# Kernel tuning notes

Hardware: AMD Instinct MI355X
Metric: run time of the kernel (lower is better)

## Reference

```python
import jax, jax.numpy as jnp
import numpy as np
from jax import lax

B, T, I, H, L = 256, 512, 156, 128, 32


def setup_inputs() -> dict:
    key = jax.random.key(0)
    ks = jax.random.split(key, 16)
    kb = 1.0 / np.sqrt(H)  # torch default LSTM/Linear init bound

    def u(k, shape, bound):
        return jax.random.uniform(k, shape, minval=-bound, maxval=bound, dtype=jnp.float32)

    return {
        "motion": jax.random.normal(ks[0], (B, T, I), dtype=jnp.float32),
        "eps": jax.random.normal(ks[1], (B, L), dtype=jnp.float32),
        # encoder LSTM (gate order i,f,g,o; b = b_ih + b_hh folded together)
        "enc_Wih": u(ks[2], (4 * H, I), kb),
        "enc_Whh": u(ks[3], (4 * H, H), kb),
        "enc_b": u(ks[4], (4 * H,), kb),
        "mu_W": u(ks[5], (L, H), kb),
        "mu_b": u(ks[6], (L,), kb),
        "var_W": u(ks[7], (L, H), kb),
        "var_b": u(ks[8], (L,), kb),
        # decoder
        "dec_fc_W": u(ks[9], (H, L), 1.0 / np.sqrt(L)),
        "dec_fc_b": u(ks[10], (H,), 1.0 / np.sqrt(L)),
        "dec_Wih": u(ks[11], (4 * H, H), kb),
        "dec_Whh": u(ks[12], (4 * H, H), kb),
        "dec_b": u(ks[13], (4 * H,), kb),
        "out_W": u(ks[14], (I, H), kb),
        "out_b": u(ks[15], (I,), kb),
    }


def _cell(gates, c):
    # PyTorch LSTM gate layout: [i, f, g, o] along the 4H axis
    i, f, g, o = jnp.split(gates, 4, axis=-1)
    c_new = jax.nn.sigmoid(f) * c + jax.nn.sigmoid(i) * jnp.tanh(g)
    h_new = jax.nn.sigmoid(o) * jnp.tanh(c_new)
    return h_new, c_new


def reference(motion, eps, enc_Wih, enc_Whh, enc_b, mu_W, mu_b, var_W, var_b,
              dec_fc_W, dec_fc_b, dec_Wih, dec_Whh, dec_b, out_W, out_b):
    b, t, _ = motion.shape

    # ---- encoder LSTM: single scan over time, keep only final hidden ----
    def enc_step(carry, x_t):
        h, c = carry
        gates = x_t @ enc_Wih.T + h @ enc_Whh.T + enc_b
        h, c = _cell(gates, c)
        return (h, c), None

    h0 = jnp.zeros((b, H), motion.dtype)
    c0 = jnp.zeros((b, H), motion.dtype)
    (h_fin, _), _ = lax.scan(enc_step, (h0, c0), jnp.swapaxes(motion, 0, 1))

    mu = h_fin @ mu_W.T + mu_b          # [B, L]
    logvar = h_fin @ var_W.T + var_b    # [B, L] ('var' in the torch code)

    # ---- reparameterize ----
    z = mu + eps * jnp.exp(0.5 * logvar)

    # ---- decoder: input at each step is the previous hidden state ----
    dh0 = z @ dec_fc_W.T + dec_fc_b     # [B, H]
    dc0 = jnp.zeros((b, H), motion.dtype)

    def dec_step(carry, _):
        h, c = carry
        gates = h @ dec_Wih.T + h @ dec_Whh.T + dec_b
        h, c = _cell(gates, c)
        return (h, c), h

    _, hs = lax.scan(dec_step, (dh0, dc0), None, length=t)  # [T, B, H]
    recon = jnp.einsum('tbh,oh->bto', hs, out_W) + out_b    # [B, T, I]

    # ---- losses ----
    rec_loss = jnp.mean((recon - motion) ** 2)
    kl_loss = -0.5 * jnp.sum(1.0 + logvar - mu ** 2 - jnp.exp(logvar))
    total = rec_loss + kl_loss
    return recon, mu, logvar, total
```

## Files before the change

kernel.cpp:

```cpp
#include <hip/hip_runtime.h>
#include <hip/hip_fp16.h>

#define B_ 256
#define T_ 512
#define I_ 156
#define H_ 128
#define L_ 32
#define G_ 512

typedef _Float16 half_t;
typedef _Float16 h2_t __attribute__((ext_vector_type(2)));

union U8 { uint4 u; h2_t h2[4]; };

__device__ __forceinline__ float fdot2(h2_t a, h2_t b, float c) {
#if __has_builtin(__builtin_amdgcn_fdot2)
  return __builtin_amdgcn_fdot2(a, b, c, false);
#else
  return c + (float)a[0] * (float)b[0] + (float)a[1] * (float)b[1];
#endif
}

__device__ __forceinline__ h2_t pk2(float a, float b) {
  h2_t r; r[0] = (half_t)a; r[1] = (half_t)b; return r;
}

__device__ __forceinline__ float sigf(float x) { return 1.0f / (1.0f + __expf(-x)); }
__device__ __forceinline__ float tanhf_(float x) {
  x = fminf(fmaxf(x, -20.f), 20.f);
  float e = __expf(2.f * x);
  return (e - 1.f) / (e + 1.f);
}

__global__ __launch_bounds__(512, 2) void enc_kernel(
    const float* __restrict__ motion, const float* __restrict__ eps,
    const float* __restrict__ Wih, const float* __restrict__ Whh,
    const float* __restrict__ bv,
    const float* __restrict__ muW, const float* __restrict__ mub,
    const float* __restrict__ varW, const float* __restrict__ varb,
    const float* __restrict__ fcW, const float* __restrict__ fcb,
    float* __restrict__ dout, float* __restrict__ dh0,
    float* __restrict__ accums)
{
  const int j = threadIdx.x;
  const int b = blockIdx.x;

  __shared__ U8 xs[20];
  __shared__ U8 hs[16];
  __shared__ float gl[G_];
  __shared__ float hf[H_];
  __shared__ float mulv[64];
  __shared__ float zs[L_];

  h2_t wih[80];
  h2_t whh[64];
  {
    const float2* r = (const float2*)(Wih + j * I_);
#pragma unroll
    for (int k = 0; k < 78; ++k) { float2 w = r[k]; wih[k] = pk2(w.x, w.y); }
    wih[78] = pk2(0.f, 0.f); wih[79] = pk2(0.f, 0.f);
    const float2* r2 = (const float2*)(Whh + j * H_);
#pragma unroll
    for (int k = 0; k < 64; ++k) { float2 w = r2[k]; whh[k] = pk2(w.x, w.y); }
  }
  const float bj = bv[j];

  float creg = 0.f, hreg = 0.f;
  if (j < 64) { ((h2_t*)hs)[j] = pk2(0.f, 0.f); }

  const float2* mrow = (const float2*)(motion + (size_t)b * T_ * I_);

  for (int t = 0; t < T_; ++t) {
    if (j < 80) {
      h2_t v = pk2(0.f, 0.f);
      if (j < 78) { float2 m = mrow[t * 78 + j]; v = pk2(m.x, m.y); }
      ((h2_t*)xs)[j] = v;
    }
    __syncthreads();
    float acc = bj;
#pragma unroll
    for (int c = 0; c < 20; ++c) {
      U8 xv = xs[c];
      acc = fdot2(wih[4*c+0], xv.h2[0], acc);
      acc = fdot2(wih[4*c+1], xv.h2[1], acc);
      acc = fdot2(wih[4*c+2], xv.h2[2], acc);
      acc = fdot2(wih[4*c+3], xv.h2[3], acc);
    }
#pragma unroll
    for (int c = 0; c < 16; ++c) {
      U8 hv = hs[c];
      acc = fdot2(whh[4*c+0], hv.h2[0], acc);
      acc = fdot2(whh[4*c+1], hv.h2[1], acc);
      acc = fdot2(whh[4*c+2], hv.h2[2], acc);
      acc = fdot2(whh[4*c+3], hv.h2[3], acc);
    }
    gl[j] = acc;
    __syncthreads();
    if (j < H_) {
      float ig = gl[j], fg = gl[j + H_], gg = gl[j + 2*H_], og = gl[j + 3*H_];
      creg = sigf(fg) * creg + sigf(ig) * tanhf_(gg);
      hreg = sigf(og) * tanhf_(creg);
      ((half_t*)hs)[j] = (half_t)hreg;
    }
    __syncthreads();
  }

  if (j < H_) hf[j] = hreg;
  __syncthreads();

  if (j < 64) {
    const float* wr = (j < L_) ? (muW + j * H_) : (varW + (j - L_) * H_);
    float a = (j < L_) ? mub[j] : varb[j - L_];
#pragma unroll 8
    for (int k = 0; k < H_; ++k) a += wr[k] * hf[k];
    mulv[j] = a;
    if (j < L_) dout[(size_t)B_*T_*I_ + b * L_ + j] = a;
    else        dout[(size_t)B_*T_*I_ + B_*L_ + b * L_ + (j - L_)] = a;
  }
  __syncthreads();

  if (j < L_) {
    float mu = mulv[j], lv = mulv[j + L_];
    float z = mu + eps[b * L_ + j] * __expf(0.5f * lv);
    zs[j] = z;
    float kt = 1.f + lv - mu * mu - __expf(lv);
#pragma unroll
    for (int off = 16; off > 0; off >>= 1) kt += __shfl_down(kt, off, 64);
    if (j == 0) atomicAdd(&accums[1], kt);
  }
  __syncthreads();

  if (j < H_) {
    const float* wr = fcW + j * L_;
    float a = fcb[j];
#pragma unroll
    for (int l = 0; l < L_; ++l) a += wr[l] * zs[l];
    dh0[b * H_ + j] = a;
  }
}

__global__ __launch_bounds__(512, 2) void dec_kernel(
    const float* __restrict__ motion,
    const float* __restrict__ Wih, const float* __restrict__ Whh,
    const float* __restrict__ bv,
    const float* __restrict__ oW, const float* __restrict__ ob,
    const float* __restrict__ dh0,
    float* __restrict__ dout, float* __restrict__ accums)
{
  const int j = threadIdx.x;
  const int b = blockIdx.x;

  __shared__ U8 hs[16];
  __shared__ float gl[G_];
  __shared__ float red[8];

  h2_t wd[64];
  {
    const float2* r1 = (const float2*)(Wih + j * H_);
    const float2* r2 = (const float2*)(Whh + j * H_);
#pragma unroll
    for (int k = 0; k < 64; ++k) {
      float2 a = r1[k], c = r2[k];
      wd[k] = pk2(a.x + c.x, a.y + c.y);
    }
  }
  const float bj = bv[j];

  h2_t wo[64];
  float obj = 0.f;
  if (j < I_) {
    const float2* r = (const float2*)(oW + j * H_);
#pragma unroll
    for (int k = 0; k < 64; ++k) { float2 w = r[k]; wo[k] = pk2(w.x, w.y); }
    obj = ob[j];
  } else {
#pragma unroll
    for (int k = 0; k < 64; ++k) wo[k] = pk2(0.f, 0.f);
  }

  float creg = 0.f, hreg = 0.f;
  if (j < H_) {
    hreg = dh0[b * H_ + j];
    ((half_t*)hs)[j] = (half_t)hreg;
  }
  __syncthreads();

  const float* mrow = motion + (size_t)b * T_ * I_;
  float* rrow = dout + (size_t)b * T_ * I_;
  float rl = 0.f;

  for (int t = 0; t < T_; ++t) {
    float acc = bj;
#pragma unroll
    for (int c = 0; c < 16; ++c) {
      U8 hv = hs[c];
      acc = fdot2(wd[4*c+0], hv.h2[0], acc);
      acc = fdot2(wd[4*c+1], hv.h2[1], acc);
      acc = fdot2(wd[4*c+2], hv.h2[2], acc);
      acc = fdot2(wd[4*c+3], hv.h2[3], acc);
    }
    gl[j] = acc;
    __syncthreads();
    if (j < H_) {
      float ig = gl[j], fg = gl[j + H_], gg = gl[j + 2*H_], og = gl[j + 3*H_];
      creg = sigf(fg) * creg + sigf(ig) * tanhf_(gg);
      hreg = sigf(og) * tanhf_(creg);
      ((half_t*)hs)[j] = (half_t)hreg;
    }
    __syncthreads();
    if (j < I_) {
      float r = obj;
#pragma unroll
      for (int c = 0; c < 16; ++c) {
        U8 hv = hs[c];
        r = fdot2(wo[4*c+0], hv.h2[0], r);
        r = fdot2(wo[4*c+1], hv.h2[1], r);
        r = fdot2(wo[4*c+2], hv.h2[2], r);
        r = fdot2(wo[4*c+3], hv.h2[3], r);
      }
      rrow[t * I_ + j] = r;
      float d = r - mrow[t * I_ + j];
      rl += d * d;
    }
  }

  float v = rl;
#pragma unroll
  for (int off = 32; off > 0; off >>= 1) v += __shfl_down(v, off, 64);
  if ((j & 63) == 0) red[j >> 6] = v;
  __syncthreads();
  if (j == 0) {
    float s = 0.f;
#pragma unroll
    for (int w = 0; w < 8; ++w) s += red[w];
    atomicAdd(&accums[0], s);
  }
}

__global__ void init_kernel(float* accums) {
  if (threadIdx.x < 2) accums[threadIdx.x] = 0.f;
}

__global__ void fin_kernel(const float* __restrict__ accums, float* __restrict__ dout) {
  if (threadIdx.x == 0) {
    float rec = accums[0] / (float)((size_t)B_ * T_ * I_);
    float kl = -0.5f * accums[1];
    dout[(size_t)B_*T_*I_ + 2 * B_ * L_] = rec + kl;
  }
}

extern "C" void kernel_launch(void* const* d_in, const int* in_sizes, int n_in,
                              void* d_out, int out_size, void* d_ws, size_t ws_size,
                              hipStream_t stream) {
  const float* motion = (const float*)d_in[0];
  const float* eps    = (const float*)d_in[1];
  const float* eWih   = (const float*)d_in[2];
  const float* eWhh   = (const float*)d_in[3];
  const float* eb     = (const float*)d_in[4];
  const float* muW    = (const float*)d_in[5];
  const float* mub    = (const float*)d_in[6];
  const float* varW   = (const float*)d_in[7];
  const float* varb   = (const float*)d_in[8];
  const float* fcW    = (const float*)d_in[9];
  const float* fcb    = (const float*)d_in[10];
  const float* dWih   = (const float*)d_in[11];
  const float* dWhh   = (const float*)d_in[12];
  const float* db     = (const float*)d_in[13];
  const float* oW     = (const float*)d_in[14];
  const float* obv    = (const float*)d_in[15];
  float* out = (float*)d_out;
  float* accums = (float*)d_ws;
  float* dh0    = (float*)d_ws + 16;

  hipLaunchKernelGGL(init_kernel, dim3(1), dim3(64), 0, stream, accums);
  hipLaunchKernelGGL(enc_kernel, dim3(B_), dim3(512), 0, stream,
                     motion, eps, eWih, eWhh, eb, muW, mub, varW, varb, fcW, fcb,
                     out, dh0, accums);
  hipLaunchKernelGGL(dec_kernel, dim3(B_), dim3(512), 0, stream,
                     motion, dWih, dWhh, db, oW, obv, dh0, out, accums);
  hipLaunchKernelGGL(fin_kernel, dim3(1), dim3(64), 0, stream, accums, out);
}
```

Measured before the change: 1.437 ms.

## Split LSTM gate dot products across 1024 threads and pipeline decoder output projection

Both kernels move to 1024-thread blocks. The encoder splits each gate's input and hidden dot products across two thread halves, sums the halves in the cell update, and prefetches the next timestep's motion row into a double buffer. The decoder gives the output projection to its own half of threads, which computes step t-1's reconstruction while the other half computes the gates for step t, taking that projection off the serial chain and removing one barrier wait per step. In exchange, launch bounds of 4 blocks of 1024 threads squeeze per-thread registers (each thread still holds 64 packed decoder weights), which risks spills or lower occupancy, and each step adds a partial-sum read through shared memory.

```diff
diff --git a/kernel.cpp b/kernel.cpp
--- a/kernel.cpp
+++ b/kernel.cpp
@@ -32,7 +32,7 @@
   return (e - 1.f) / (e + 1.f);
 }
 
-__global__ __launch_bounds__(512, 2) void enc_kernel(
+__global__ __launch_bounds__(1024, 4) void enc_kernel(
     const float* __restrict__ motion, const float* __restrict__ eps,
     const float* __restrict__ Wih, const float* __restrict__ Whh,
     const float* __restrict__ bv,
@@ -42,104 +42,125 @@
     float* __restrict__ dout, float* __restrict__ dh0,
     float* __restrict__ accums)
 {
-  const int j = threadIdx.x;
-  const int b = blockIdx.x;
-
-  __shared__ U8 xs[20];
-  __shared__ U8 hs[16];
-  __shared__ float gl[G_];
+  const int tid  = threadIdx.x;
+  const int part = tid >> 9;
+  const int j    = tid & 511;
+  const int b    = blockIdx.x;
+
+  __shared__ h2_t xs[2][80];
+  __shared__ h2_t hs[64];
+  __shared__ float gl2[2][G_];
   __shared__ float hf[H_];
   __shared__ float mulv[64];
   __shared__ float zs[L_];
 
-  h2_t wih[80];
-  h2_t whh[64];
+  h2_t wih[40];
+  h2_t whh[32];
   {
-    const float2* r = (const float2*)(Wih + j * I_);
-#pragma unroll
-    for (int k = 0; k < 78; ++k) { float2 w = r[k]; wih[k] = pk2(w.x, w.y); }
-    wih[78] = pk2(0.f, 0.f); wih[79] = pk2(0.f, 0.f);
-    const float2* r2 = (const float2*)(Whh + j * H_);
-#pragma unroll
-    for (int k = 0; k < 64; ++k) { float2 w = r2[k]; whh[k] = pk2(w.x, w.y); }
-  }
-  const float bj = bv[j];
+    const int cbase = part * 80;
+    const float* wr = Wih + (size_t)j * I_;
+#pragma unroll
+    for (int k = 0; k < 40; ++k) {
+      int c0 = cbase + 2 * k;
+      float a = (c0     < I_) ? wr[c0]     : 0.f;
+      float c = (c0 + 1 < I_) ? wr[c0 + 1] : 0.f;
+      wih[k] = pk2(a, c);
+    }
+    const float2* r2 = (const float2*)(Whh + (size_t)j * H_ + part * 64);
+#pragma unroll
+    for (int k = 0; k < 32; ++k) { float2 w = r2[k]; whh[k] = pk2(w.x, w.y); }
+  }
+
+  float cb0 = 0.f, cb1 = 0.f, cb2 = 0.f, cb3 = 0.f;
+  if (tid < H_) {
+    cb0 = bv[tid]; cb1 = bv[tid + H_]; cb2 = bv[tid + 2*H_]; cb3 = bv[tid + 3*H_];
+  }
 
   float creg = 0.f, hreg = 0.f;
-  if (j < 64) { ((h2_t*)hs)[j] = pk2(0.f, 0.f); }
+  if (tid < 64) hs[tid] = pk2(0.f, 0.f);
+  if (tid < 4)  xs[tid >> 1][78 + (tid & 1)] = pk2(0.f, 0.f);
 
   const float2* mrow = (const float2*)(motion + (size_t)b * T_ * I_);
-
+  const bool loader = (part == 1) && (j < 78);
+  if (loader) { float2 m = mrow[j]; xs[0][j] = pk2(m.x, m.y); }
+  __syncthreads();
+
+  int cur = 0;
+  float2 xreg;
   for (int t = 0; t < T_; ++t) {
-    if (j < 80) {
-      h2_t v = pk2(0.f, 0.f);
-      if (j < 78) { float2 m = mrow[t * 78 + j]; v = pk2(m.x, m.y); }
-      ((h2_t*)xs)[j] = v;
-    }
+    if (loader && t + 1 < T_) xreg = mrow[(t + 1) * 78 + j];
+
+    float a0 = 0.f, a1 = 0.f, a2 = 0.f, a3 = 0.f;
+    const U8* xv = (const U8*)&xs[cur][part * 40];
+#pragma unroll
+    for (int c = 0; c < 10; ++c) {
+      U8 v = xv[c];
+      a0 = fdot2(wih[4*c+0], v.h2[0], a0);
+      a1 = fdot2(wih[4*c+1], v.h2[1], a1);
+      a2 = fdot2(wih[4*c+2], v.h2[2], a2);
+      a3 = fdot2(wih[4*c+3], v.h2[3], a3);
+    }
+    const U8* hv = (const U8*)&hs[part * 32];
+#pragma unroll
+    for (int c = 0; c < 8; ++c) {
+      U8 v = hv[c];
+      a0 = fdot2(whh[4*c+0], v.h2[0], a0);
+      a1 = fdot2(whh[4*c+1], v.h2[1], a1);
+      a2 = fdot2(whh[4*c+2], v.h2[2], a2);
+      a3 = fdot2(whh[4*c+3], v.h2[3], a3);
+    }
+    gl2[part][j] = (a0 + a1) + (a2 + a3);
+    if (loader && t + 1 < T_) xs[cur ^ 1][j] = pk2(xreg.x, xreg.y);
     __syncthreads();
-    float acc = bj;
-#pragma unroll
-    for (int c = 0; c < 20; ++c) {
-      U8 xv = xs[c];
-      acc = fdot2(wih[4*c+0], xv.h2[0], acc);
-      acc = fdot2(wih[4*c+1], xv.h2[1], acc);
-      acc = fdot2(wih[4*c+2], xv.h2[2], acc);
-      acc = fdot2(wih[4*c+3], xv.h2[3], acc);
-    }
-#pragma unroll
-    for (int c = 0; c < 16; ++c) {
-      U8 hv = hs[c];
-      acc = fdot2(whh[4*c+0], hv.h2[0], acc);
-      acc = fdot2(whh[4*c+1], hv.h2[1], acc);
-      acc = fdot2(whh[4*c+2], hv.h2[2], acc);
-      acc = fdot2(whh[4*c+3], hv.h2[3], acc);
-    }
-    gl[j] = acc;
-    __syncthreads();
-    if (j < H_) {
-      float ig = gl[j], fg = gl[j + H_], gg = gl[j + 2*H_], og = gl[j + 3*H_];
+
+    if (tid < H_) {
+      float ig = gl2[0][tid]         + gl2[1][tid]         + cb0;
+      float fg = gl2[0][tid +   H_]  + gl2[1][tid +   H_]  + cb1;
+      float gg = gl2[0][tid + 2*H_]  + gl2[1][tid + 2*H_]  + cb2;
+      float og = gl2[0][tid + 3*H_]  + gl2[1][tid + 3*H_]  + cb3;
       creg = sigf(fg) * creg + sigf(ig) * tanhf_(gg);
       hreg = sigf(og) * tanhf_(creg);
-      ((half_t*)hs)[j] = (half_t)hreg;
+      ((half_t*)hs)[tid] = (half_t)hreg;
     }
     __syncthreads();
-  }
-
-  if (j < H_) hf[j] = hreg;
-  __syncthreads();
-
-  if (j < 64) {
-    const float* wr = (j < L_) ? (muW + j * H_) : (varW + (j - L_) * H_);
-    float a = (j < L_) ? mub[j] : varb[j - L_];
+    cur ^= 1;
+  }
+
+  if (tid < H_) hf[tid] = hreg;
+  __syncthreads();
+
+  if (tid < 64) {
+    const float* wr = (tid < L_) ? (muW + tid * H_) : (varW + (tid - L_) * H_);
+    float a = (tid < L_) ? mub[tid] : varb[tid - L_];
 #pragma unroll 8
     for (int k = 0; k < H_; ++k) a += wr[k] * hf[k];
-    mulv[j] = a;
-    if (j < L_) dout[(size_t)B_*T_*I_ + b * L_ + j] = a;
-    else        dout[(size_t)B_*T_*I_ + B_*L_ + b * L_ + (j - L_)] = a;
-  }
-  __syncthreads();
-
-  if (j < L_) {
-    float mu = mulv[j], lv = mulv[j + L_];
-    float z = mu + eps[b * L_ + j] * __expf(0.5f * lv);
-    zs[j] = z;
+    mulv[tid] = a;
+    if (tid < L_) dout[(size_t)B_*T_*I_ + b * L_ + tid] = a;
+    else          dout[(size_t)B_*T_*I_ + B_*L_ + b * L_ + (tid - L_)] = a;
+  }
+  __syncthreads();
+
+  if (tid < L_) {
+    float mu = mulv[tid], lv = mulv[tid + L_];
+    float z = mu + eps[b * L_ + tid] * __expf(0.5f * lv);
+    zs[tid] = z;
     float kt = 1.f + lv - mu * mu - __expf(lv);
 #pragma unroll
     for (int off = 16; off > 0; off >>= 1) kt += __shfl_down(kt, off, 64);
-    if (j == 0) atomicAdd(&accums[1], kt);
-  }
-  __syncthreads();
-
-  if (j < H_) {
-    const float* wr = fcW + j * L_;
-    float a = fcb[j];
+    if (tid == 0) atomicAdd(&accums[1], kt);
+  }
+  __syncthreads();
+
+  if (tid < H_) {
+    const float* wr = fcW + tid * L_;
+    float a = fcb[tid];
 #pragma unroll
     for (int l = 0; l < L_; ++l) a += wr[l] * zs[l];
-    dh0[b * H_ + j] = a;
-  }
-}
-
-__global__ __launch_bounds__(512, 2) void dec_kernel(
+    dh0[b * H_ + tid] = a;
+  }
+}
+
+__global__ __launch_bounds__(1024, 4) void dec_kernel(
     const float* __restrict__ motion,
     const float* __restrict__ Wih, const float* __restrict__ Whh,
     const float* __restrict__ bv,
@@ -147,92 +168,110 @@
     const float* __restrict__ dh0,
     float* __restrict__ dout, float* __restrict__ accums)
 {
-  const int j = threadIdx.x;
-  const int b = blockIdx.x;
-
-  __shared__ U8 hs[16];
+  const int tid  = threadIdx.x;
+  const int part = tid >> 9;
+  const int j    = tid & 511;
+  const int b    = blockIdx.x;
+
+  __shared__ h2_t hs[64];
   __shared__ float gl[G_];
-  __shared__ float red[8];
-
-  h2_t wd[64];
-  {
-    const float2* r1 = (const float2*)(Wih + j * H_);
-    const float2* r2 = (const float2*)(Whh + j * H_);
+  __shared__ float red[16];
+
+  h2_t wv[64];
+  float bj = 0.f;
+  if (part == 0) {
+    const float2* r1 = (const float2*)(Wih + (size_t)j * H_);
+    const float2* r2 = (const float2*)(Whh + (size_t)j * H_);
 #pragma unroll
     for (int k = 0; k < 64; ++k) {
       float2 a = r1[k], c = r2[k];
-      wd[k] = pk2(a.x + c.x, a.y + c.y);
-    }
-  }
-  const float bj = bv[j];
-
-  h2_t wo[64];
-  float obj = 0.f;
-  if (j < I_) {
-    const float2* r = (const float2*)(oW + j * H_);
-#pragma unroll
-    for (int k = 0; k < 64; ++k) { float2 w = r[k]; wo[k] = pk2(w.x, w.y); }
-    obj = ob[j];
-  } else {
-#pragma unroll
-    for (int k = 0; k < 64; ++k) wo[k] = pk2(0.f, 0.f);
+      wv[k] = pk2(a.x + c.x, a.y + c.y);
+    }
+    bj = bv[j];
+  } else if (j < I_) {
+    const float2* r = (const float2*)(oW + (size_t)j * H_);
+#pragma unroll
+    for (int k = 0; k < 64; ++k) { float2 w = r[k]; wv[k] = pk2(w.x, w.y); }
+    bj = ob[j];
   }
 
   float creg = 0.f, hreg = 0.f;
-  if (j < H_) {
-    hreg = dh0[b * H_ + j];
-    ((half_t*)hs)[j] = (half_t)hreg;
-  }
-  __syncthreads();
-
-  const float* mrow = motion + (size_t)b * T_ * I_;
-  float* rrow = dout + (size_t)b * T_ * I_;
+  if (tid < H_) {
+    hreg = dh0[b * H_ + tid];
+    ((half_t*)hs)[tid] = (half_t)hreg;
+  }
+  __syncthreads();
+
+  const float* mr = motion + (size_t)b * T_ * I_;
+  float* rr = dout + (size_t)b * T_ * I_;
   float rl = 0.f;
 
   for (int t = 0; t < T_; ++t) {
-    float acc = bj;
-#pragma unroll
-    for (int c = 0; c < 16; ++c) {
-      U8 hv = hs[c];
-      acc = fdot2(wd[4*c+0], hv.h2[0], acc);
-      acc = fdot2(wd[4*c+1], hv.h2[1], acc);
-      acc = fdot2(wd[4*c+2], hv.h2[2], acc);
-      acc = fdot2(wd[4*c+3], hv.h2[3], acc);
-    }
-    gl[j] = acc;
+    if (part == 0) {
+      float a0 = 0.f, a1 = 0.f, a2 = 0.f, a3 = 0.f;
+      const U8* hv = (const U8*)hs;
+#pragma unroll
+      for (int c = 0; c < 16; ++c) {
+        U8 v = hv[c];
+        a0 = fdot2(wv[4*c+0], v.h2[0], a0);
+        a1 = fdot2(wv[4*c+1], v.h2[1], a1);
+        a2 = fdot2(wv[4*c+2], v.h2[2], a2);
+        a3 = fdot2(wv[4*c+3], v.h2[3], a3);
+      }
+      gl[j] = bj + (a0 + a1) + (a2 + a3);
+    } else if (j < I_ && t > 0) {
+      float a0 = 0.f, a1 = 0.f, a2 = 0.f, a3 = 0.f;
+      const U8* hv = (const U8*)hs;
+#pragma unroll
+      for (int c = 0; c < 16; ++c) {
+        U8 v = hv[c];
+        a0 = fdot2(wv[4*c+0], v.h2[0], a0);
+        a1 = fdot2(wv[4*c+1], v.h2[1], a1);
+        a2 = fdot2(wv[4*c+2], v.h2[2], a2);
+        a3 = fdot2(wv[4*c+3], v.h2[3], a3);
+      }
+      float r = bj + (a0 + a1) + (a2 + a3);
+      rr[(t - 1) * I_ + j] = r;
+      float d = r - mr[(t - 1) * I_ + j];
+      rl += d * d;
+    }
     __syncthreads();
-    if (j < H_) {
-      float ig = gl[j], fg = gl[j + H_], gg = gl[j + 2*H_], og = gl[j + 3*H_];
+
+    if (tid < H_) {
+      float ig = gl[tid], fg = gl[tid + H_], gg = gl[tid + 2*H_], og = gl[tid + 3*H_];
       creg = sigf(fg) * creg + sigf(ig) * tanhf_(gg);
       hreg = sigf(og) * tanhf_(creg);
-      ((half_t*)hs)[j] = (half_t)hreg;
+      ((half_t*)hs)[tid] = (half_t)hreg;
     }
     __syncthreads();
-    if (j < I_) {
-      float r = obj;
-#pragma unroll
-      for (int c = 0; c < 16; ++c) {
-        U8 hv = hs[c];
-        r = fdot2(wo[4*c+0], hv.h2[0], r);
-        r = fdot2(wo[4*c+1], hv.h2[1], r);
-        r = fdot2(wo[4*c+2], hv.h2[2], r);
-        r = fdot2(wo[4*c+3], hv.h2[3], r);
-      }
-      rrow[t * I_ + j] = r;
-      float d = r - mrow[t * I_ + j];
-      rl += d * d;
-    }
+  }
+
+  if (part == 1 && j < I_) {
+    float a0 = 0.f, a1 = 0.f, a2 = 0.f, a3 = 0.f;
+    const U8* hv = (const U8*)hs;
+#pragma unroll
+    for (int c = 0; c < 16; ++c) {
+      U8 v = hv[c];
+      a0 = fdot2(wv[4*c+0], v.h2[0], a0);
+      a1 = fdot2(wv[4*c+1], v.h2[1], a1);
+      a2 = fdot2(wv[4*c+2], v.h2[2], a2);
+      a3 = fdot2(wv[4*c+3], v.h2[3], a3);
+    }
+    float r = bj + (a0 + a1) + (a2 + a3);
+    rr[511 * I_ + j] = r;
+    float d = r - mr[511 * I_ + j];
+    rl += d * d;
   }
 
   float v = rl;
 #pragma unroll
   for (int off = 32; off > 0; off >>= 1) v += __shfl_down(v, off, 64);
-  if ((j & 63) == 0) red[j >> 6] = v;
-  __syncthreads();
-  if (j == 0) {
+  if ((tid & 63) == 0) red[tid >> 6] = v;
+  __syncthreads();
+  if (tid == 0) {
     float s = 0.f;
 #pragma unroll
-    for (int w = 0; w < 8; ++w) s += red[w];
+    for (int w = 0; w < 16; ++w) s += red[w];
     atomicAdd(&accums[0], s);
   }
 }
@@ -273,10 +312,10 @@
   float* dh0    = (float*)d_ws + 16;
 
   hipLaunchKernelGGL(init_kernel, dim3(1), dim3(64), 0, stream, accums);
-  hipLaunchKernelGGL(enc_kernel, dim3(B_), dim3(512), 0, stream,
+  hipLaunchKernelGGL(enc_kernel, dim3(B_), dim3(1024), 0, stream,
                      motion, eps, eWih, eWhh, eb, muW, mub, varW, varb, fcW, fcb,
                      out, dh0, accums);
-  hipLaunchKernelGGL(dec_kernel, dim3(B_), dim3(512), 0, stream,
+  hipLaunchKernelGGL(dec_kernel, dim3(B_), dim3(1024), 0, stream,
                      motion, dWih, dWhh, db, oW, obv, dh0, out, accums);
   hipLaunchKernelGGL(fin_kernel, dim3(1), dim3(64), 0, stream, accums, out);
 }
```

Measured after the change: 1.162 ms. 1.24x faster.
